# Kernel tuning notes

Hardware: AMD Instinct MI355X
Metric: run time of the kernel (lower is better)

Reference implementation:

```python
import jax, jax.numpy as jnp
import numpy as np

N_NODES = 50000
N_EDGES = 800000
IN_CH, HID, OUT_CH, EDGE_DIM = 256, 128, 64, 64
NUM_LAYERS = 3


def _linear_init(key, fan_in, fan_out):
    # torch nn.Linear default: U(-1/sqrt(fan_in), 1/sqrt(fan_in))
    kw, kb = jax.random.split(key)
    bound = 1.0 / np.sqrt(fan_in)
    W = jax.random.uniform(kw, (fan_in, fan_out), minval=-bound, maxval=bound, dtype=jnp.float32)
    b = jax.random.uniform(kb, (fan_out,), minval=-bound, maxval=bound, dtype=jnp.float32)
    return W, b


def setup_inputs() -> dict:
    key = jax.random.key(0)
    ks = jax.random.split(key, 8)
    x = jax.random.normal(ks[0], (N_NODES, IN_CH), dtype=jnp.float32)
    edge_index = jax.random.randint(ks[1], (2, N_EDGES), 0, N_NODES, dtype=jnp.int64)
    edge_attr = jax.random.normal(ks[2], (N_EDGES, EDGE_DIM), dtype=jnp.float32)
    W_in, b_in = _linear_init(ks[3], IN_CH, HID)
    W_e, b_e = _linear_init(ks[4], EDGE_DIM, HID)
    W1, b1 = _linear_init(ks[5], HID, HID)
    W2, b2 = _linear_init(ks[6], HID, HID)
    W_out, b_out = _linear_init(ks[7], HID, OUT_CH)
    return {"x": x, "edge_index": edge_index, "edge_attr": edge_attr,
            "W_in": W_in, "b_in": b_in, "W_e": W_e, "b_e": b_e,
            "W1": W1, "b1": b1, "W2": W2, "b2": b2,
            "W_out": W_out, "b_out": b_out}


def reference(x, edge_index, edge_attr, W_in, b_in, W_e, b_e, W1, b1, W2, b2, W_out, b_out):
    N = x.shape[0]
    src, dst = edge_index[0], edge_index[1]
    # input projection (in_channels != hidden_channels)
    h = x @ W_in + b_in                      # [N, HID]
    # edge projection is layer-independent (shared GINEConv weights)
    e = edge_attr @ W_e + b_e                # [E, HID]
    for _ in range(NUM_LAYERS):
        # GINEConv: message = relu(h_src + e), sum-aggregate to dst, eps=0
        msg = jax.nn.relu(h[src] + e)        # [E, HID]
        agg = jax.ops.segment_sum(msg, dst, num_segments=N)
        z = h + agg                          # (1+eps)*h + agg, eps=0
        # conv nn: MLP Linear->relu->Linear (plain_last)
        z = jax.nn.relu(z @ W1 + b1) @ W2 + b2
        # outer act
        h = jax.nn.relu(z)
    return h @ W_out + b_out                 # [N, OUT_CH]
```

## Files before the change

### kernel.cpp

```cpp
#include <hip/hip_runtime.h>
#include <hip/hip_bf16.h>
#include <stdint.h>

#define N_NODES 50000
#define N_EDGES 800000
#define IN_CH 256
#define HID 128
#define OUT_CH 64
#define EDGE_DIM 64

#define AGG_EW  64
#define AGG_CAP 128
#define AGG_B   (N_EDGES / AGG_EW)
#define SCB     196

typedef __hip_bfloat16 bf16;
typedef __attribute__((ext_vector_type(8))) short short8;
typedef __attribute__((ext_vector_type(4))) float f32x4;

__device__ __forceinline__ void st_out(float* p, float v) { *p = v; }
__device__ __forceinline__ void st_out(bf16* p, float v) { *p = __float2bfloat16(v); }

__device__ __forceinline__ void wt_one(const float* W, bf16* Wt, int K, int N, int i) {
    int n = i % N, k = i / N;
    Wt[n * K + k] = __float2bfloat16(W[i]);
}
__launch_bounds__(256)
__global__ void wt_prep_all(const float* W_in, const float* W_e, const float* W1,
                            const float* W2, const float* W_out,
                            bf16* Wt_in, bf16* Wt_e, bf16* Wt_1, bf16* Wt_2, bf16* Wt_out) {
    int i = blockIdx.x * 256 + threadIdx.x;
    if (i < 32768)       wt_one(W_in,  Wt_in,  256, 128, i);
    else if (i < 40960)  wt_one(W_e,   Wt_e,    64, 128, i - 32768);
    else if (i < 57344)  wt_one(W1,    Wt_1,   128, 128, i - 40960);
    else if (i < 73728)  wt_one(W2,    Wt_2,   128, 128, i - 57344);
    else if (i < 81920)  wt_one(W_out, Wt_out, 128,  64, i - 73728);
}

template<int KTOT, int N, int MROWS, bool RELU, typename InT, typename OutT>
__launch_bounds__(256)
__global__ void gemm_mfma(const InT* __restrict__ A, const bf16* __restrict__ Wt,
                          const float* __restrict__ b, OutT* __restrict__ out, int M) {
    static_assert(KTOT % 64 == 0, "");
    constexpr int KC  = 64;
    constexpr int NCH = KTOT / KC;
    constexpr int KCP = KC + 8;
    constexpr int NT  = N / 16;
    constexpr int MT  = MROWS / 64;
    __shared__ __align__(16) bf16 Ws[N * KCP];
    __shared__ __align__(16) bf16 As[MROWS * KCP];

    const int tid  = threadIdx.x;
    const int wave = tid >> 6;
    const int lane = tid & 63;
    const int quad = lane >> 4;
    const int l16  = lane & 15;
    const int base = blockIdx.x * MROWS;

    f32x4 acc[MT][NT];
    #pragma unroll
    for (int m = 0; m < MT; m++)
        #pragma unroll
        for (int i = 0; i < NT; i++) acc[m][i] = (f32x4){0.f, 0.f, 0.f, 0.f};

    for (int ch = 0; ch < NCH; ch++) {
        const int kc = ch * KC;
        constexpr int WIT = N * KC / (256 * 8);
        #pragma unroll
        for (int it = 0; it < WIT; it++) {
            int t8 = (it * 256 + tid) * 8;
            int n = t8 / KC, k = t8 % KC;
            *(uint4*)&Ws[n * KCP + k] = *(const uint4*)&Wt[n * KTOT + kc + k];
        }
        if constexpr (sizeof(InT) == 4) {
            constexpr int AIT = MROWS * KC / (256 * 4);
            #pragma unroll
            for (int it = 0; it < AIT; it++) {
                int t4 = (it * 256 + tid) * 4;
                int r = t4 / KC, k = t4 % KC;
                int gr = base + r;
                float4 v = (gr < M) ? *(const float4*)&A[(size_t)gr * KTOT + kc + k]
                                    : make_float4(0.f, 0.f, 0.f, 0.f);
                *(__hip_bfloat162*)&As[r * KCP + k]     = __float22bfloat162_rn(make_float2(v.x, v.y));
                *(__hip_bfloat162*)&As[r * KCP + k + 2] = __float22bfloat162_rn(make_float2(v.z, v.w));
            }
        } else {
            constexpr int AIT = MROWS * KC / (256 * 8);
            #pragma unroll
            for (int it = 0; it < AIT; it++) {
                int t8 = (it * 256 + tid) * 8;
                int r = t8 / KC, k = t8 % KC;
                int gr = base + r;
                uint4 v = (gr < M) ? *(const uint4*)&A[(size_t)gr * KTOT + kc + k]
                                   : make_uint4(0u, 0u, 0u, 0u);
                *(uint4*)&As[r * KCP + k] = v;
            }
        }
        __syncthreads();

        #pragma unroll
        for (int ks = 0; ks < KC / 32; ks++) {
            short8 af[MT];
            #pragma unroll
            for (int m = 0; m < MT; m++)
                af[m] = *(const short8*)&As[(wave * MT * 16 + m * 16 + l16) * KCP + ks * 32 + quad * 8];
            #pragma unroll
            for (int nt = 0; nt < NT; nt++) {
                short8 bfr = *(const short8*)&Ws[(nt * 16 + l16) * KCP + ks * 32 + quad * 8];
                #pragma unroll
                for (int m = 0; m < MT; m++)
                    acc[m][nt] = __builtin_amdgcn_mfma_f32_16x16x32_bf16(af[m], bfr, acc[m][nt], 0, 0, 0);
            }
        }
        __syncthreads();
    }

    #pragma unroll
    for (int m = 0; m < MT; m++) {
        const int r0 = base + wave * MT * 16 + m * 16 + quad * 4;
        #pragma unroll
        for (int reg = 0; reg < 4; reg++) {
            int gr = r0 + reg;
            if (gr < M) {
                #pragma unroll
                for (int nt = 0; nt < NT; nt++) {
                    int col = nt * 16 + l16;
                    float v = acc[m][nt][reg] + b[col];
                    if (RELU) v = fmaxf(v, 0.f);
                    st_out(&out[(size_t)gr * N + col], v);
                }
            }
        }
    }
}

__launch_bounds__(256)
__global__ void hist_kernel(const int* __restrict__ ei, int* __restrict__ counts) {
    int edge = blockIdx.x * 256 + threadIdx.x;
    if (edge < N_EDGES) atomicAdd(&counts[ei[N_EDGES + edge]], 1);
}

__launch_bounds__(256)
__global__ void scan_a(const int* __restrict__ counts, int* __restrict__ bsum) {
    __shared__ int sh[256];
    const int tid = threadIdx.x;
    int n = blockIdx.x * 256 + tid;
    sh[tid] = (n < N_NODES) ? counts[n] : 0;
    __syncthreads();
    for (int off = 128; off > 0; off >>= 1) {
        if (tid < off) sh[tid] += sh[tid + off];
        __syncthreads();
    }
    if (tid == 0) bsum[blockIdx.x] = sh[0];
}

__launch_bounds__(256)
__global__ void scan_b(const int* __restrict__ bsum, int* __restrict__ bpre) {
    __shared__ int sh[256];
    const int tid = threadIdx.x;
    int v = (tid < SCB) ? bsum[tid] : 0;
    sh[tid] = v;
    __syncthreads();
    for (int off = 1; off < 256; off <<= 1) {
        int t = (tid >= off) ? sh[tid - off] : 0;
        __syncthreads();
        sh[tid] += t;
        __syncthreads();
    }
    if (tid < SCB) bpre[tid] = sh[tid] - v;
}

__launch_bounds__(256)
__global__ void scan_c(const int* __restrict__ counts, const int* __restrict__ bpre,
                       int* __restrict__ offsets, int* __restrict__ cursor) {
    __shared__ int sh[256];
    const int tid = threadIdx.x;
    int n = blockIdx.x * 256 + tid;
    int c = (n < N_NODES) ? counts[n] : 0;
    sh[tid] = c;
    __syncthreads();
    for (int off = 1; off < 256; off <<= 1) {
        int t = (tid >= off) ? sh[tid - off] : 0;
        __syncthreads();
        sh[tid] += t;
        __syncthreads();
    }
    if (n < N_NODES) {
        int excl = bpre[blockIdx.x] + sh[tid] - c;
        offsets[n] = excl;
        cursor[n]  = excl;
    }
    if (blockIdx.x == 0 && tid == 0) offsets[N_NODES] = N_EDGES;
}

__launch_bounds__(256)
__global__ void scan_d(const int* __restrict__ offsets, int* __restrict__ blkstart) {
    int n = blockIdx.x * 256 + threadIdx.x;
    if (n > N_NODES) return;
    int v = (n == N_NODES) ? N_EDGES : offsets[n];
    int lo = 0;
    if (n > 0) lo = offsets[n - 1] / AGG_EW + 1;
    int hi = v / AGG_EW;
    for (int bb = lo; bb <= hi; bb++) blkstart[bb] = n;
    if (n == N_NODES) blkstart[AGG_B + 1] = N_NODES;
}

__launch_bounds__(256)
__global__ void scatter_perm(const int* __restrict__ ei, int* __restrict__ cursor,
                             int* __restrict__ poe, int* __restrict__ srcs) {
    int edge = blockIdx.x * 256 + threadIdx.x;
    if (edge >= N_EDGES) return;
    int dst = ei[N_EDGES + edge];
    int pos = atomicAdd(&cursor[dst], 1);
    poe[edge] = pos;
    srcs[pos] = ei[edge];
}

__launch_bounds__(256)
__global__ void ea_permute(const float* __restrict__ ea, const int* __restrict__ poe,
                           bf16* __restrict__ eas) {
    int t = blockIdx.x * 256 + threadIdx.x;
    int edge = t >> 4, l16 = t & 15;
    if (edge >= N_EDGES) return;
    float4 v = *(const float4*)&ea[(size_t)edge * EDGE_DIM + l16 * 4];
    int pos = poe[edge];
    __hip_bfloat162 p0 = __float22bfloat162_rn(make_float2(v.x, v.y));
    __hip_bfloat162 p1 = __float22bfloat162_rn(make_float2(v.z, v.w));
    uint2 u = make_uint2(*(uint32_t*)&p0, *(uint32_t*)&p1);
    *(uint2*)&eas[(size_t)pos * EDGE_DIM + l16 * 4] = u;
}

__device__ __forceinline__ float blo(uint32_t u) { return __uint_as_float(u << 16); }
__device__ __forceinline__ float bhi(uint32_t u) { return __uint_as_float(u & 0xffff0000u); }

__launch_bounds__(256)
__global__ void agg_fused(const int* __restrict__ offsets, const int* __restrict__ blkstart,
                          const int* __restrict__ srcs, const bf16* __restrict__ eas,
                          const bf16* __restrict__ Wt_e, const float* __restrict__ b_e,
                          const bf16* __restrict__ h, bf16* __restrict__ z) {
    constexpr int P = 136;
    __shared__ __align__(16) bf16 et[AGG_CAP * P];
    __shared__ int srcs_s[AGG_CAP];

    const int b    = blockIdx.x;
    const int tid  = threadIdx.x;
    const int wave = tid >> 6;
    const int lane = tid & 63;
    const int quad = lane >> 4;
    const int l16  = lane & 15;

    const int n0 = blkstart[b], n1 = blkstart[b + 1];
    if (n0 >= n1) return;
    const int e0 = offsets[n0];
    int e1 = offsets[n1];
    if (e1 > e0 + AGG_CAP) e1 = e0 + AGG_CAP;
    const int ne = e1 - e0;

    if (tid < AGG_CAP) srcs_s[tid] = (tid < ne) ? srcs[e0 + tid] : 0;

    short8 af[2][2];
    float4 bias[2];
    #pragma unroll
    for (int ct = 0; ct < 2; ct++) {
        int chr = (wave * 2 + ct) * 16 + l16;
        #pragma unroll
        for (int ks = 0; ks < 2; ks++)
            af[ct][ks] = *(const short8*)&Wt_e[chr * EDGE_DIM + ks * 32 + quad * 8];
        bias[ct] = *(const float4*)&b_e[(wave * 2 + ct) * 16 + quad * 4];
    }
    const int nsub = (ne + 15) >> 4;
    for (int es = 0; es < nsub; es++) {
        int erow = es * 16 + l16;
        int ge = e0 + erow;
        short8 bf0 = (short8){0,0,0,0,0,0,0,0}, bf1 = bf0;
        if (erow < ne) {
            bf0 = *(const short8*)&eas[(size_t)ge * EDGE_DIM + quad * 8];
            bf1 = *(const short8*)&eas[(size_t)ge * EDGE_DIM + 32 + quad * 8];
        }
        #pragma unroll
        for (int ct = 0; ct < 2; ct++) {
            f32x4 acc = (f32x4){0.f, 0.f, 0.f, 0.f};
            acc = __builtin_amdgcn_mfma_f32_16x16x32_bf16(af[ct][0], bf0, acc, 0, 0, 0);
            acc = __builtin_amdgcn_mfma_f32_16x16x32_bf16(af[ct][1], bf1, acc, 0, 0, 0);
            int row = es * 16 + l16;
            int ch0 = (wave * 2 + ct) * 16 + quad * 4;
            __hip_bfloat162 p0 = __float22bfloat162_rn(make_float2(acc[0] + bias[ct].x, acc[1] + bias[ct].y));
            __hip_bfloat162 p1 = __float22bfloat162_rn(make_float2(acc[2] + bias[ct].z, acc[3] + bias[ct].w));
            *(uint2*)&et[row * P + ch0] = make_uint2(*(uint32_t*)&p0, *(uint32_t*)&p1);
        }
    }
    __syncthreads();

    const int c = lane * 2;
    for (int n = n0 + wave; n < n1; n += 4) {
        int s  = offsets[n] - e0;
        int ee = offsets[n + 1] - e0;
        if (ee > ne) ee = ne;
        float2 a = make_float2(0.f, 0.f);
        int i = s;
        for (; i + 3 < ee; i += 4) {
            int s0 = srcs_s[i], s1 = srcs_s[i + 1], s2 = srcs_s[i + 2], s3 = srcs_s[i + 3];
            uint32_t ev0 = *(const uint32_t*)&et[(i + 0) * P + c];
            uint32_t ev1 = *(const uint32_t*)&et[(i + 1) * P + c];
            uint32_t ev2 = *(const uint32_t*)&et[(i + 2) * P + c];
            uint32_t ev3 = *(const uint32_t*)&et[(i + 3) * P + c];
            uint32_t h0 = *(const uint32_t*)&h[(size_t)s0 * HID + c];
            uint32_t h1 = *(const uint32_t*)&h[(size_t)s1 * HID + c];
            uint32_t h2 = *(const uint32_t*)&h[(size_t)s2 * HID + c];
            uint32_t h3 = *(const uint32_t*)&h[(size_t)s3 * HID + c];
            a.x += fmaxf(blo(h0) + blo(ev0), 0.f);
            a.y += fmaxf(bhi(h0) + bhi(ev0), 0.f);
            a.x += fmaxf(blo(h1) + blo(ev1), 0.f);
            a.y += fmaxf(bhi(h1) + bhi(ev1), 0.f);
            a.x += fmaxf(blo(h2) + blo(ev2), 0.f);
            a.y += fmaxf(bhi(h2) + bhi(ev2), 0.f);
            a.x += fmaxf(blo(h3) + blo(ev3), 0.f);
            a.y += fmaxf(bhi(h3) + bhi(ev3), 0.f);
        }
        for (; i < ee; i++) {
            int s0 = srcs_s[i];
            uint32_t ev0 = *(const uint32_t*)&et[i * P + c];
            uint32_t h0 = *(const uint32_t*)&h[(size_t)s0 * HID + c];
            a.x += fmaxf(blo(h0) + blo(ev0), 0.f);
            a.y += fmaxf(bhi(h0) + bhi(ev0), 0.f);
        }
        uint32_t hn = *(const uint32_t*)&h[(size_t)n * HID + c];
        a.x += blo(hn);
        a.y += bhi(hn);
        __hip_bfloat162 p = __float22bfloat162_rn(make_float2(a.x, a.y));
        *(uint32_t*)&z[(size_t)n * HID + c] = *(uint32_t*)&p;
    }
}

extern "C" void kernel_launch(void* const* d_in, const int* in_sizes, int n_in,
                              void* d_out, int out_size, void* d_ws, size_t ws_size,
                              hipStream_t stream) {
    const float* x     = (const float*)d_in[0];
    const int*   ei    = (const int*)d_in[1];
    const float* ea    = (const float*)d_in[2];
    const float* W_in  = (const float*)d_in[3];
    const float* b_in  = (const float*)d_in[4];
    const float* W_e   = (const float*)d_in[5];
    const float* b_e   = (const float*)d_in[6];
    const float* W1    = (const float*)d_in[7];
    const float* b1    = (const float*)d_in[8];
    const float* W2    = (const float*)d_in[9];
    const float* b2    = (const float*)d_in[10];
    const float* W_out = (const float*)d_in[11];
    const float* b_out = (const float*)d_in[12];
    float* out = (float*)d_out;

    char* ws = (char*)d_ws;
    size_t off = 0;
    bf16*  h        = (bf16*) (ws + off); off += (size_t)N_NODES * HID * 2;
    bf16*  z        = (bf16*) (ws + off); off += (size_t)N_NODES * HID * 2;
    bf16*  eas      = (bf16*) (ws + off); off += (size_t)N_EDGES * EDGE_DIM * 2;
    int*   counts   = (int*)  (ws + off); off += (size_t)N_NODES * 4;
    int*   offsets  = (int*)  (ws + off); off += (size_t)(N_NODES + 1) * 4;
    int*   cursor   = (int*)  (ws + off); off += (size_t)N_NODES * 4;
    int*   poe      = (int*)  (ws + off); off += (size_t)N_EDGES * 4;
    int*   srcs     = (int*)  (ws + off); off += (size_t)N_EDGES * 4;
    int*   blkstart = (int*)  (ws + off); off += (size_t)(AGG_B + 2) * 4;
    int*   bsum     = (int*)  (ws + off); off += (size_t)SCB * 4;
    int*   bpre     = (int*)  (ws + off); off += (size_t)SCB * 4;
    bf16*  Wt_in    = (bf16*) (ws + off); off += (size_t)HID * IN_CH * 2;
    bf16*  Wt_e     = (bf16*) (ws + off); off += (size_t)HID * EDGE_DIM * 2;
    bf16*  Wt_1     = (bf16*) (ws + off); off += (size_t)HID * HID * 2;
    bf16*  Wt_2     = (bf16*) (ws + off); off += (size_t)HID * HID * 2;
    bf16*  Wt_out   = (bf16*) (ws + off); off += (size_t)OUT_CH * HID * 2;

    wt_prep_all<<<(81920 + 255) / 256, 256, 0, stream>>>(
        W_in, W_e, W1, W2, W_out, Wt_in, Wt_e, Wt_1, Wt_2, Wt_out);

    hipMemsetAsync(counts, 0, (size_t)N_NODES * 4, stream);
    hist_kernel<<<(N_EDGES + 255) / 256, 256, 0, stream>>>(ei, counts);
    scan_a<<<SCB, 256, 0, stream>>>(counts, bsum);
    scan_b<<<1, 256, 0, stream>>>(bsum, bpre);
    scan_c<<<SCB, 256, 0, stream>>>(counts, bpre, offsets, cursor);
    scan_d<<<SCB, 256, 0, stream>>>(offsets, blkstart);
    scatter_perm<<<(N_EDGES + 255) / 256, 256, 0, stream>>>(ei, cursor, poe, srcs);

    ea_permute<<<(N_EDGES * 16 + 255) / 256, 256, 0, stream>>>(ea, poe, eas);

    gemm_mfma<IN_CH, HID, 64, false, float, bf16>
        <<<(N_NODES + 63) / 64, 256, 0, stream>>>(x, Wt_in, b_in, h, N_NODES);

    for (int layer = 0; layer < 3; ++layer) {
        agg_fused<<<AGG_B + 1, 256, 0, stream>>>(offsets, blkstart, srcs, eas, Wt_e, b_e, h, z);
        gemm_mfma<HID, HID, 64, true, bf16, bf16>
            <<<(N_NODES + 63) / 64, 256, 0, stream>>>(z, Wt_1, b1, h, N_NODES);
        gemm_mfma<HID, HID, 64, true, bf16, bf16>
            <<<(N_NODES + 63) / 64, 256, 0, stream>>>(h, Wt_2, b2, z, N_NODES);
        bf16* t = h; h = z; z = t;
    }

    gemm_mfma<HID, OUT_CH, 64, false, bf16, float>
        <<<(N_NODES + 63) / 64, 256, 0, stream>>>(h, Wt_out, b_out, out, N_NODES);
}
```

Before: 884.7 us.

## Vectorize edge gather to 16-byte loads across quads and prefetch edge attrs

The aggregation loop now has each wave process four edges at once: each quad of 16 lanes handles one edge, loading 8 bf16 channels per lane with 16-byte loads. Partial sums are then reduced across quads with shuffles. The edge-projection loop also software-prefetches the next 16-row tile of edge attributes while the MFMAs run on the current one. This cuts the number of narrow gather instructions and hides global load latency, at the cost of shuffle reductions, idle quads when a node has fewer than four edges, and more registers. The srcs_s array is padded by four entries.

```diff
diff --git a/kernel.cpp b/kernel.cpp
--- a/kernel.cpp
+++ b/kernel.cpp
@@ -240,7 +240,7 @@
                           const bf16* __restrict__ h, bf16* __restrict__ z) {
     constexpr int P = 136;
     __shared__ __align__(16) bf16 et[AGG_CAP * P];
-    __shared__ int srcs_s[AGG_CAP];
+    __shared__ int srcs_s[AGG_CAP + 4];
 
     const int b    = blockIdx.x;
     const int tid  = threadIdx.x;
@@ -256,7 +256,7 @@
     if (e1 > e0 + AGG_CAP) e1 = e0 + AGG_CAP;
     const int ne = e1 - e0;
 
-    if (tid < AGG_CAP) srcs_s[tid] = (tid < ne) ? srcs[e0 + tid] : 0;
+    if (tid < AGG_CAP + 4) srcs_s[tid] = (tid < ne) ? srcs[e0 + tid] : 0;
 
     short8 af[2][2];
     float4 bias[2];
@@ -269,66 +269,73 @@
         bias[ct] = *(const float4*)&b_e[(wave * 2 + ct) * 16 + quad * 4];
     }
     const int nsub = (ne + 15) >> 4;
+    short8 cb0 = (short8){0,0,0,0,0,0,0,0}, cb1 = cb0;
+    if (l16 < ne) {
+        cb0 = *(const short8*)&eas[(size_t)(e0 + l16) * EDGE_DIM + quad * 8];
+        cb1 = *(const short8*)&eas[(size_t)(e0 + l16) * EDGE_DIM + 32 + quad * 8];
+    }
     for (int es = 0; es < nsub; es++) {
-        int erow = es * 16 + l16;
-        int ge = e0 + erow;
-        short8 bf0 = (short8){0,0,0,0,0,0,0,0}, bf1 = bf0;
-        if (erow < ne) {
-            bf0 = *(const short8*)&eas[(size_t)ge * EDGE_DIM + quad * 8];
-            bf1 = *(const short8*)&eas[(size_t)ge * EDGE_DIM + 32 + quad * 8];
+        short8 nb0 = (short8){0,0,0,0,0,0,0,0}, nb1 = nb0;
+        int nrow = (es + 1) * 16 + l16;
+        if (nrow < ne) {
+            nb0 = *(const short8*)&eas[(size_t)(e0 + nrow) * EDGE_DIM + quad * 8];
+            nb1 = *(const short8*)&eas[(size_t)(e0 + nrow) * EDGE_DIM + 32 + quad * 8];
         }
         #pragma unroll
         for (int ct = 0; ct < 2; ct++) {
             f32x4 acc = (f32x4){0.f, 0.f, 0.f, 0.f};
-            acc = __builtin_amdgcn_mfma_f32_16x16x32_bf16(af[ct][0], bf0, acc, 0, 0, 0);
-            acc = __builtin_amdgcn_mfma_f32_16x16x32_bf16(af[ct][1], bf1, acc, 0, 0, 0);
+            acc = __builtin_amdgcn_mfma_f32_16x16x32_bf16(af[ct][0], cb0, acc, 0, 0, 0);
+            acc = __builtin_amdgcn_mfma_f32_16x16x32_bf16(af[ct][1], cb1, acc, 0, 0, 0);
             int row = es * 16 + l16;
             int ch0 = (wave * 2 + ct) * 16 + quad * 4;
             __hip_bfloat162 p0 = __float22bfloat162_rn(make_float2(acc[0] + bias[ct].x, acc[1] + bias[ct].y));
             __hip_bfloat162 p1 = __float22bfloat162_rn(make_float2(acc[2] + bias[ct].z, acc[3] + bias[ct].w));
             *(uint2*)&et[row * P + ch0] = make_uint2(*(uint32_t*)&p0, *(uint32_t*)&p1);
         }
+        cb0 = nb0; cb1 = nb1;
     }
     __syncthreads();
 
-    const int c = lane * 2;
+    const int c8 = l16 * 8;
     for (int n = n0 + wave; n < n1; n += 4) {
         int s  = offsets[n] - e0;
         int ee = offsets[n + 1] - e0;
         if (ee > ne) ee = ne;
-        float2 a = make_float2(0.f, 0.f);
-        int i = s;
-        for (; i + 3 < ee; i += 4) {
-            int s0 = srcs_s[i], s1 = srcs_s[i + 1], s2 = srcs_s[i + 2], s3 = srcs_s[i + 3];
-            uint32_t ev0 = *(const uint32_t*)&et[(i + 0) * P + c];
-            uint32_t ev1 = *(const uint32_t*)&et[(i + 1) * P + c];
-            uint32_t ev2 = *(const uint32_t*)&et[(i + 2) * P + c];
-            uint32_t ev3 = *(const uint32_t*)&et[(i + 3) * P + c];
-            uint32_t h0 = *(const uint32_t*)&h[(size_t)s0 * HID + c];
-            uint32_t h1 = *(const uint32_t*)&h[(size_t)s1 * HID + c];
-            uint32_t h2 = *(const uint32_t*)&h[(size_t)s2 * HID + c];
-            uint32_t h3 = *(const uint32_t*)&h[(size_t)s3 * HID + c];
-            a.x += fmaxf(blo(h0) + blo(ev0), 0.f);
-            a.y += fmaxf(bhi(h0) + bhi(ev0), 0.f);
-            a.x += fmaxf(blo(h1) + blo(ev1), 0.f);
-            a.y += fmaxf(bhi(h1) + bhi(ev1), 0.f);
-            a.x += fmaxf(blo(h2) + blo(ev2), 0.f);
-            a.y += fmaxf(bhi(h2) + bhi(ev2), 0.f);
-            a.x += fmaxf(blo(h3) + blo(ev3), 0.f);
-            a.y += fmaxf(bhi(h3) + bhi(ev3), 0.f);
-        }
-        for (; i < ee; i++) {
-            int s0 = srcs_s[i];
-            uint32_t ev0 = *(const uint32_t*)&et[i * P + c];
-            uint32_t h0 = *(const uint32_t*)&h[(size_t)s0 * HID + c];
-            a.x += fmaxf(blo(h0) + blo(ev0), 0.f);
-            a.y += fmaxf(bhi(h0) + bhi(ev0), 0.f);
-        }
-        uint32_t hn = *(const uint32_t*)&h[(size_t)n * HID + c];
-        a.x += blo(hn);
-        a.y += bhi(hn);
-        __hip_bfloat162 p = __float22bfloat162_rn(make_float2(a.x, a.y));
-        *(uint32_t*)&z[(size_t)n * HID + c] = *(uint32_t*)&p;
+        float a[8];
+        #pragma unroll
+        for (int j = 0; j < 8; j++) a[j] = 0.f;
+        for (int i = s; i < ee; i += 4) {
+            int idx = i + quad;
+            if (idx < ee) {
+                int src = srcs_s[idx];
+                uint4 hv = *(const uint4*)&h[(size_t)src * HID + c8];
+                uint4 ev = *(const uint4*)&et[idx * P + c8];
+                uint32_t hs[4] = {hv.x, hv.y, hv.z, hv.w};
+                uint32_t vs[4] = {ev.x, ev.y, ev.z, ev.w};
+                #pragma unroll
+                for (int j = 0; j < 4; j++) {
+                    a[2 * j]     += fmaxf(blo(hs[j]) + blo(vs[j]), 0.f);
+                    a[2 * j + 1] += fmaxf(bhi(hs[j]) + bhi(vs[j]), 0.f);
+                }
+            }
+        }
+        #pragma unroll
+        for (int j = 0; j < 8; j++) {
+            a[j] += __shfl_xor(a[j], 16);
+            a[j] += __shfl_xor(a[j], 32);
+        }
+        if (lane < 16) {
+            uint4 hn = *(const uint4*)&h[(size_t)n * HID + c8];
+            uint32_t hs[4] = {hn.x, hn.y, hn.z, hn.w};
+            uint32_t o[4];
+            #pragma unroll
+            for (int j = 0; j < 4; j++) {
+                __hip_bfloat162 p = __float22bfloat162_rn(
+                    make_float2(a[2 * j] + blo(hs[j]), a[2 * j + 1] + bhi(hs[j])));
+                o[j] = *(uint32_t*)&p;
+            }
+            *(uint4*)&z[(size_t)n * HID + c8] = make_uint4(o[0], o[1], o[2], o[3]);
+        }
     }
 }
 
```

Measured after the change: 902.9 us. 1.02x slower.
